# Performance work log

Hardware: AMD Instinct MI355X
Metric: run time of the kernel (lower is better)

The kernel has to match this reference:

```python
import jax
import jax.numpy as jnp
import numpy as np

N_NODES = 4096
N_EDGES = 65536
D_FEAT = 64


def setup_inputs() -> dict:
    key = jax.random.key(0)
    k1, k2, k3, k4 = jax.random.split(key, 4)
    x = jax.random.normal(k1, (N_NODES, D_FEAT), dtype=jnp.float32)
    edge_index = jax.random.randint(k2, (2, N_EDGES), 0, N_NODES, dtype=jnp.int32)
    batch = jnp.zeros((N_NODES,), dtype=jnp.int32)
    # GraphConv(in_channels, 1): lin_rel (with bias) on aggregated neighbors, lin_root on self
    w_rel = jax.random.normal(k3, (D_FEAT, 1), dtype=jnp.float32) * 0.1
    w_root = jax.random.normal(k4, (D_FEAT, 1), dtype=jnp.float32) * 0.1
    b = jnp.zeros((1,), dtype=jnp.float32)
    return {"x": x, "edge_index": edge_index, "batch": batch,
            "w_rel": w_rel, "w_root": w_root, "b": b}


def _merge_stars(x, src0, dst0, score):
    """Faithful sequential greedy star contraction (priority order by score desc)."""
    N = x.shape[0]
    order = jnp.argsort(-score)  # descending, ties like argsort

    def step(carry, node):
        xc, src, dst, remaining, center = carry
        active = remaining[node]
        # dests = set of targets of edges whose (current, rewritten) source == node,
        # minus already-chosen center nodes
        dest_edge = src == node                                  # [E]
        dest_node = jnp.zeros(N, bool).at[dst].max(dest_edge)    # node-level set
        dest_node = dest_node & ~center
        # torch does sum over list(dests)+[node]: node counted again (even on self-loop)
        combine = jnp.einsum('n,nd->d', dest_node.astype(xc.dtype), xc) + xc[node]
        D = dest_node.at[node].set(True)                         # dests U {node}
        x2 = xc.at[node].set(combine)
        src2 = jnp.where(D[src], node, src)                      # np.isin rewrite
        dst2 = jnp.where(D[dst], node, dst)
        rem2 = remaining & ~dest_node
        cen2 = center.at[node].set(True)
        carry2 = (jnp.where(active, x2, xc),
                  jnp.where(active, src2, src),
                  jnp.where(active, dst2, dst),
                  jnp.where(active, rem2, remaining),
                  jnp.where(active, cen2, center))
        return carry2, None

    init = (x, src0, dst0, jnp.ones(N, bool), jnp.zeros(N, bool))
    (x_final, _, _, remaining, _), _ = jax.lax.scan(step, init, order)
    return x_final, remaining


def reference(x, edge_index, batch, w_rel, w_root, b):
    N, d = x.shape
    src0, dst0 = edge_index[0], edge_index[1]
    # GraphConv score: W_rel * sum_{j->i} x_j + b + W_root * x_i ; dropout p=0; tanh
    agg = jax.ops.segment_sum(x[src0], dst0, num_segments=N)     # [N, d]
    score = jnp.tanh((agg @ w_rel + x @ w_root + b).reshape(-1)) # [N]

    x_final, remaining = _merge_stars(x, src0, dst0, score)

    # perm = sorted(nodes_remaining); outputs padded to static size N (sentinel -1)
    perm = jnp.nonzero(remaining, size=N, fill_value=N)[0]
    x_pooled = jnp.take(x_final, perm, axis=0, mode='fill', fill_value=0.0)
    kept = perm < N
    batch_pooled = jnp.where(kept, jnp.take(batch, jnp.minimum(perm, N - 1)), -1)
    # filter_adj on the ORIGINAL edge_index: keep edges with both endpoints kept,
    # relabel nodes to their rank among kept nodes; invalid edges -> -1
    relabel = jnp.cumsum(remaining.astype(jnp.int32)) - 1
    valid = remaining[src0] & remaining[dst0]
    new_src = jnp.where(valid, relabel[src0], -1)
    new_dst = jnp.where(valid, relabel[dst0], -1)
    new_edge_index = jnp.stack([new_src, new_dst])
    perm_out = jnp.where(kept, perm, -1)
    return x_pooled, new_edge_index, batch_pooled, perm_out
```

## Files before the change

kernel.cpp:

```cpp
#include <hip/hip_runtime.h>

#define NN 4096
#define NE 65536
#define ND 64


__global__ void k1_dots_count(const float* __restrict__ x, const float* __restrict__ wrel,
                              const float* __restrict__ wroot, const int* __restrict__ ei,
                              double* __restrict__ srel, double* __restrict__ sroot,
                              int* __restrict__ cnt) {
    int gt = blockIdx.x * blockDim.x + threadIdx.x;
    int node = gt >> 6, lane = gt & 63;
    double xv = (double)x[gt];
    double pr = xv * (double)wrel[lane];
    double po = xv * (double)wroot[lane];
    for (int off = 32; off > 0; off >>= 1) {
        pr += __shfl_down(pr, off);
        po += __shfl_down(po, off);
    }
    if (lane == 0) {
        srel[node] = pr;
        sroot[node] = po;
    }
    if (gt < NE / 4) {
        const int4* eid4 = (const int4*)(ei + NE);
        int4 q = eid4[gt];
        atomicAdd(&cnt[q.x], 1);
        atomicAdd(&cnt[q.y], 1);
        atomicAdd(&cnt[q.z], 1);
        atomicAdd(&cnt[q.w], 1);
    }
}

__global__ void __launch_bounds__(1024) k2_scan(const int* __restrict__ cnt,
                                                int* __restrict__ rowst,
                                                int* __restrict__ cursor) {
    __shared__ int wt[16];
    int tid = threadIdx.x, lane = tid & 63, wv = tid >> 6;
    int4 c = ((const int4*)cnt)[tid];
    int tot = c.x + c.y + c.z + c.w;
    int inc = tot;
    for (int off = 1; off < 64; off <<= 1) {
        int v = __shfl_up(inc, off);
        if (lane >= off) inc += v;
    }
    if (lane == 63) wt[wv] = inc;
    __syncthreads();
    if (wv == 0 && lane < 16) {
        int v = wt[lane];
        for (int off = 1; off < 16; off <<= 1) {
            int u2 = __shfl_up(v, off);
            if (lane >= off) v += u2;
        }
        wt[lane] = v;
    }
    __syncthreads();
    int waveoff = (wv > 0) ? wt[wv - 1] : 0;
    int excl = waveoff + inc - tot;
    int4 rs;
    rs.x = excl; rs.y = excl + c.x; rs.z = excl + c.x + c.y; rs.w = excl + c.x + c.y + c.z;
    ((int4*)rowst)[tid] = rs;
    ((int4*)cursor)[tid] = rs;
    if (tid == 0) rowst[NN] = NE;
}

__global__ void k3_scatter(const int* __restrict__ ei, int* __restrict__ cursor,
                           unsigned short* __restrict__ incsr) {
    int i = blockIdx.x * blockDim.x + threadIdx.x;
    const int4* eis4 = (const int4*)ei;
    const int4* eid4 = (const int4*)(ei + NE);
    int4 s = eis4[i];
    int4 d = eid4[i];
    incsr[atomicAdd(&cursor[d.x], 1)] = (unsigned short)s.x;
    incsr[atomicAdd(&cursor[d.y], 1)] = (unsigned short)s.y;
    incsr[atomicAdd(&cursor[d.z], 1)] = (unsigned short)s.z;
    incsr[atomicAdd(&cursor[d.w], 1)] = (unsigned short)s.w;
}

__global__ void k4_keys(const double* __restrict__ srel, const double* __restrict__ sroot,
                        const float* __restrict__ bptr, const int* __restrict__ rowst,
                        const unsigned short* __restrict__ incsr, unsigned* __restrict__ key) {
    int v = blockIdx.x * blockDim.x + threadIdx.x;
    int rs = rowst[v], re = rowst[v + 1];
    double s = 0.0;
    for (int e = rs; e < re; ++e) s += srel[(int)incsr[e]];
    double arg = s + sroot[v] + (double)bptr[0];
    float sc = tanhf((float)arg);
    unsigned m = __float_as_uint(sc);
    m = (m & 0x80000000u) ? ~m : (m | 0x80000000u);
    key[v] = m;
}

__global__ void k5_filtersort(const int* __restrict__ rowst, const unsigned* __restrict__ key,
                              unsigned short* __restrict__ incsr, int* __restrict__ rl,
                              float* __restrict__ out) {
    int g = blockIdx.x * blockDim.x + threadIdx.x;
    if (g < (NN * ND) / 4) ((float4*)out)[g] = make_float4(0.f, 0.f, 0.f, 0.f);

    int v = g >> 6, l = g & 63;
    int rs = rowst[v], deg = rowst[v + 1] - rs;
    unsigned mv = key[v];
    if (deg <= 64) {
        int u = (l < deg) ? (int)incsr[rs + l] : -1;
        bool isself = (l < deg) && (u == v);
        unsigned mu = (l < deg && !isself) ? key[u] : 0u;
        bool keep = (l < deg) && !isself && (mu > mv || (mu == mv && u < v));
        unsigned long long val = keep
            ? ((((unsigned long long)(~mu)) << 12) | (unsigned)u) : ~0ULL;
        int m = __popcll(__ballot(keep));
        bool selfAny = __ballot(isself) != 0ULL;
        for (int k = 2; k <= 64; k <<= 1) {
            for (int j = k >> 1; j > 0; j >>= 1) {
                unsigned long long o = __shfl_xor(val, j);
                bool takeMin = ((l & k) == 0) == ((l & j) == 0);
                unsigned long long mn = (o < val) ? o : val;
                unsigned long long mx = (o < val) ? val : o;
                val = takeMin ? mn : mx;
            }
        }
        if (l < m) incsr[rs + l] = (unsigned short)(val & 0xFFFULL);
        if (l == 0) rl[v] = m | (selfAny ? 0x10000 : 0);
    } else if (l == 0) {
        int w = rs;
        bool selfAny = false;
        for (int e = rs; e < rs + deg; ++e) {
            int u = (int)incsr[e];
            if (u == v) { selfAny = true; continue; }
            unsigned mu = key[u];
            if (!(mu > mv || (mu == mv && u < v))) continue;
            int j = w;
            while (j > rs) {
                int q = (int)incsr[j - 1];
                unsigned mq = key[q];
                if (mu > mq || (mu == mq && u < q)) { incsr[j] = (unsigned short)q; --j; }
                else break;
            }
            incsr[j] = (unsigned short)u; ++w;
        }
        rl[v] = (w - rs) | (selfAny ? 0x10000 : 0);
    }
}

__global__ void __launch_bounds__(1024) k34_fix(
        const int* __restrict__ rowst, const int* __restrict__ rl,
        const unsigned short* __restrict__ incsr_g,
        int* __restrict__ map_g, int* __restrict__ rem_g, int* __restrict__ relab_g,
        int* __restrict__ perm_a, int* __restrict__ nkeep_g) {
    __shared__ __align__(16) char buf[135232];
    unsigned short* incsr = (unsigned short*)buf;
    volatile unsigned char* stat = (volatile unsigned char*)(buf + 131072);
    int* wt = (int*)(buf + 135168);
    int tid = threadIdx.x, lane = tid & 63, wv = tid >> 6;

    for (int i = tid; i < 131072 / 16; i += 1024)
        ((int4*)incsr)[i] = ((const int4*)incsr_g)[i];
    ((int*)(buf + 131072))[tid] = 0;
    int4 rsq = ((const int4*)rowst)[tid];
    int4 rlq = ((const int4*)rl)[tid];
    int rs4[4] = {rsq.x, rsq.y, rsq.z, rsq.w};
    int rq4[4] = {rlq.x, rlq.y, rlq.z, rlq.w};
    __syncthreads();

    unsigned resolved = 0, centerm = 0, selfm = 0;
    int pos4[4], re4[4], fu4[4] = {0, 0, 0, 0};
    #pragma unroll
    for (int t = 0; t < 4; ++t) {
        int v = 4 * tid + t;
        int m = rq4[t] & 0xFFFF;
        if (rq4[t] & 0x10000) selfm |= 1u << t;
        int lo = rs4[t];
        pos4[t] = lo; re4[t] = lo + m;
        if (m == 0) {
            map_g[v] = v; stat[v] = 1;
            centerm |= 1u << t; resolved |= 1u << t;
        } else {
            fu4[t] = (int)incsr[lo];
        }
    }

    int guard = 0;
    while (resolved != 0xFu && guard < 1000000) {
        ++guard;
        bool prog = false;
        #pragma unroll
        for (int t = 0; t < 4; ++t) {
            if (resolved & (1u << t)) continue;
            int v = 4 * tid + t;
            int u = fu4[t];
            int st = (int)stat[u];
            if (st == 0) continue;
            prog = true;
            if (st == 1) {
                map_g[v] = u; stat[v] = 2; resolved |= 1u << t; continue;
            }
            int p = pos4[t] + 1, hi = re4[t];
            bool done = false;
            while (p < hi) {
                u = (int)incsr[p];
                st = (int)stat[u];
                if (st == 2) { ++p; continue; }
                if (st == 1) {
                    map_g[v] = u; stat[v] = 2; resolved |= 1u << t; done = true;
                }
                break;
            }
            if (!done) {
                if (p >= hi) {
                    map_g[v] = v; stat[v] = 1; centerm |= 1u << t; resolved |= 1u << t;
                } else {
                    pos4[t] = p; fu4[t] = u;
                }
            }
        }
        if (__ballot(prog) == 0) __builtin_amdgcn_s_sleep(1);
    }
    __syncthreads();

    int remb[4], cnt4 = 0;
    #pragma unroll
    for (int t = 0; t < 4; ++t) {
        remb[t] = ((centerm >> t) & 1) && !((selfm >> t) & 1);
        cnt4 += remb[t];
    }
    int inc2 = cnt4;
    for (int off = 1; off < 64; off <<= 1) {
        int v = __shfl_up(inc2, off);
        if (lane >= off) inc2 += v;
    }
    if (lane == 63) wt[wv] = inc2;
    __syncthreads();
    if (wv == 0 && lane < 16) {
        int v = wt[lane];
        for (int off = 1; off < 16; off <<= 1) {
            int u2 = __shfl_up(v, off);
            if (lane >= off) v += u2;
        }
        wt[lane] = v;
    }
    __syncthreads();
    int woff2 = (wv > 0) ? wt[wv - 1] : 0;
    int run = woff2 + inc2 - cnt4;
    #pragma unroll
    for (int t = 0; t < 4; ++t) {
        int v = 4 * tid + t;
        relab_g[v] = run;
        if (remb[t]) { perm_a[run] = v; ++run; }
        rem_g[v] = remb[t];
    }
    if (tid == 1023) nkeep_g[0] = run;
}

__global__ void k56_outputs(const float* __restrict__ x, const int* __restrict__ map_g,
                            const int* __restrict__ rem_g, const int* __restrict__ relab_g,
                            const int* __restrict__ perm_a, const int* __restrict__ ei,
                            const int* __restrict__ batch, const int* __restrict__ nkeep_g,
                            float* __restrict__ out) {
    int idx = blockIdx.x * blockDim.x + threadIdx.x;
    if (idx < NN * ND) {
        int n = idx >> 6, d = idx & 63;
        int m = map_g[n];
        if (rem_g[m]) atomicAdd(&out[relab_g[m] * ND + d], x[idx]);
    } else if (idx < NN * ND + 2 * NE) {
        int e = idx - NN * ND;
        int row = e >> 16;
        int ee = e & (NE - 1);
        int s = ei[ee], t = ei[NE + ee];
        bool valid = (rem_g[s] != 0) && (rem_g[t] != 0);
        int endp = (row == 0) ? s : t;
        out[idx] = valid ? (float)relab_g[endp] : -1.0f;
    } else if (idx < NN * ND + 2 * NE + NN) {
        int r = idx - (NN * ND + 2 * NE);
        int nk = nkeep_g[0];
        out[idx] = (r < nk) ? (float)batch[perm_a[r]] : -1.0f;
    } else if (idx < NN * ND + 2 * NE + 2 * NN) {
        int r = idx - (NN * ND + 2 * NE + NN);
        int nk = nkeep_g[0];
        out[idx] = (r < nk) ? (float)perm_a[r] : -1.0f;
    }
}

extern "C" void kernel_launch(void* const* d_in, const int* in_sizes, int n_in,
                              void* d_out, int out_size, void* d_ws, size_t ws_size,
                              hipStream_t stream) {
    const float* x     = (const float*)d_in[0];
    const int*   ei    = (const int*)d_in[1];
    const int*   batch = (const int*)d_in[2];
    const float* wrel  = (const float*)d_in[3];
    const float* wroot = (const float*)d_in[4];
    const float* b     = (const float*)d_in[5];

    char* ws = (char*)d_ws;
    double* srel   = (double*)(ws + 0);
    double* sroot  = (double*)(ws + 32768);
    int*    map_g  = (int*)(ws + 65536);
    int*    rem_g  = (int*)(ws + 81920);
    int*    relab  = (int*)(ws + 98304);
    int*    perma  = (int*)(ws + 114688);
    int*    nkeep  = (int*)(ws + 131072);
    int*    cnt    = (int*)(ws + 131136);
    int*    rowst  = (int*)(ws + 147520);
    int*    cursor = (int*)(ws + 163968);
    unsigned short* incsr = (unsigned short*)(ws + 180352);
    int*      rl  = cnt;
    unsigned* key = (unsigned*)cursor;

    float* out = (float*)d_out;

    hipMemsetAsync(cnt, 0, NN * sizeof(int), stream);
    k1_dots_count<<<NN * ND / 256, 256, 0, stream>>>(x, wrel, wroot, ei, srel, sroot, cnt);
    k2_scan<<<1, 1024, 0, stream>>>(cnt, rowst, cursor);
    k3_scatter<<<(NE / 4) / 256, 256, 0, stream>>>(ei, cursor, incsr);
    k4_keys<<<NN / 256, 256, 0, stream>>>(srel, sroot, b, rowst, incsr, key);
    k5_filtersort<<<(NN * 64) / 256, 256, 0, stream>>>(rowst, key, incsr, rl, out);
    k34_fix<<<1, 1024, 0, stream>>>(rowst, rl, incsr, map_g, rem_g, relab, perma, nkeep);
    int total_out = NN * ND + 2 * NE + 2 * NN;
    k56_outputs<<<(total_out + 255) / 256, 256, 0, stream>>>(x, map_g, rem_g, relab,
                                                             perma, ei, batch, nkeep, out);
}
```

Before: 139.7 us.

## Build CSR in one LDS-resident block and compute keys by aggregating features

Replaces the memset, count, scan and scatter kernels with a single 1024-thread block that counts, scans and scatters entirely in LDS (about 144 KB) before copying the CSR to global memory. The score kernel now sums neighbour feature rows directly with one wave per node, then dots the sum with the weights, so the separate per-node dot-product pass is no longer needed. This removes several launches and global atomics, but serialises CSR construction onto one CU and makes the key pass read a 64-float row for every edge.

```diff
diff --git a/kernel.cpp b/kernel.cpp
--- a/kernel.cpp
+++ b/kernel.cpp
@@ -5,40 +5,30 @@
 #define ND 64
 
 
-__global__ void k1_dots_count(const float* __restrict__ x, const float* __restrict__ wrel,
-                              const float* __restrict__ wroot, const int* __restrict__ ei,
-                              double* __restrict__ srel, double* __restrict__ sroot,
-                              int* __restrict__ cnt) {
-    int gt = blockIdx.x * blockDim.x + threadIdx.x;
-    int node = gt >> 6, lane = gt & 63;
-    double xv = (double)x[gt];
-    double pr = xv * (double)wrel[lane];
-    double po = xv * (double)wroot[lane];
-    for (int off = 32; off > 0; off >>= 1) {
-        pr += __shfl_down(pr, off);
-        po += __shfl_down(po, off);
-    }
-    if (lane == 0) {
-        srel[node] = pr;
-        sroot[node] = po;
-    }
-    if (gt < NE / 4) {
-        const int4* eid4 = (const int4*)(ei + NE);
-        int4 q = eid4[gt];
-        atomicAdd(&cnt[q.x], 1);
-        atomicAdd(&cnt[q.y], 1);
-        atomicAdd(&cnt[q.z], 1);
-        atomicAdd(&cnt[q.w], 1);
-    }
-}
-
-__global__ void __launch_bounds__(1024) k2_scan(const int* __restrict__ cnt,
-                                                int* __restrict__ rowst,
-                                                int* __restrict__ cursor) {
-    __shared__ int wt[16];
+__global__ void __launch_bounds__(1024) kB_csr(const int* __restrict__ ei,
+                                               unsigned short* __restrict__ incsr_g,
+                                               int* __restrict__ rowst_g) {
+    __shared__ __align__(16) char buf[147520];
+    unsigned short* incsr = (unsigned short*)buf;
+    int* cursor = (int*)(buf + 131072);
+    int* wt = (int*)(buf + 147456);
     int tid = threadIdx.x, lane = tid & 63, wv = tid >> 6;
-    int4 c = ((const int4*)cnt)[tid];
-    int tot = c.x + c.y + c.z + c.w;
+
+    for (int n = tid; n < NN; n += 1024) cursor[n] = 0;
+    __syncthreads();
+    const int4* eid4 = (const int4*)(ei + NE);
+    for (int i = tid; i < NE / 4; i += 1024) {
+        int4 q = eid4[i];
+        atomicAdd(&cursor[q.x], 1);
+        atomicAdd(&cursor[q.y], 1);
+        atomicAdd(&cursor[q.z], 1);
+        atomicAdd(&cursor[q.w], 1);
+    }
+    __syncthreads();
+
+    int t0 = cursor[4 * tid], t1 = cursor[4 * tid + 1];
+    int t2 = cursor[4 * tid + 2], t3 = cursor[4 * tid + 3];
+    int tot = t0 + t1 + t2 + t3;
     int inc = tot;
     for (int off = 1; off < 64; off <<= 1) {
         int v = __shfl_up(inc, off);
@@ -57,38 +47,56 @@
     __syncthreads();
     int waveoff = (wv > 0) ? wt[wv - 1] : 0;
     int excl = waveoff + inc - tot;
-    int4 rs;
-    rs.x = excl; rs.y = excl + c.x; rs.z = excl + c.x + c.y; rs.w = excl + c.x + c.y + c.z;
-    ((int4*)rowst)[tid] = rs;
-    ((int4*)cursor)[tid] = rs;
-    if (tid == 0) rowst[NN] = NE;
-}
-
-__global__ void k3_scatter(const int* __restrict__ ei, int* __restrict__ cursor,
-                           unsigned short* __restrict__ incsr) {
-    int i = blockIdx.x * blockDim.x + threadIdx.x;
+    int4 rsv;
+    rsv.x = excl; rsv.y = excl + t0; rsv.z = excl + t0 + t1; rsv.w = excl + t0 + t1 + t2;
+    ((int4*)rowst_g)[tid] = rsv;
+    if (tid == 1023) rowst_g[NN] = NE;
+    cursor[4 * tid]     = rsv.x;
+    cursor[4 * tid + 1] = rsv.y;
+    cursor[4 * tid + 2] = rsv.z;
+    cursor[4 * tid + 3] = rsv.w;
+    __syncthreads();
+
     const int4* eis4 = (const int4*)ei;
-    const int4* eid4 = (const int4*)(ei + NE);
-    int4 s = eis4[i];
-    int4 d = eid4[i];
-    incsr[atomicAdd(&cursor[d.x], 1)] = (unsigned short)s.x;
-    incsr[atomicAdd(&cursor[d.y], 1)] = (unsigned short)s.y;
-    incsr[atomicAdd(&cursor[d.z], 1)] = (unsigned short)s.z;
-    incsr[atomicAdd(&cursor[d.w], 1)] = (unsigned short)s.w;
-}
-
-__global__ void k4_keys(const double* __restrict__ srel, const double* __restrict__ sroot,
-                        const float* __restrict__ bptr, const int* __restrict__ rowst,
-                        const unsigned short* __restrict__ incsr, unsigned* __restrict__ key) {
-    int v = blockIdx.x * blockDim.x + threadIdx.x;
-    int rs = rowst[v], re = rowst[v + 1];
-    double s = 0.0;
-    for (int e = rs; e < re; ++e) s += srel[(int)incsr[e]];
-    double arg = s + sroot[v] + (double)bptr[0];
-    float sc = tanhf((float)arg);
-    unsigned m = __float_as_uint(sc);
-    m = (m & 0x80000000u) ? ~m : (m | 0x80000000u);
-    key[v] = m;
+    for (int i = tid; i < NE / 4; i += 1024) {
+        int4 s = eis4[i];
+        int4 d = eid4[i];
+        incsr[atomicAdd(&cursor[d.x], 1)] = (unsigned short)s.x;
+        incsr[atomicAdd(&cursor[d.y], 1)] = (unsigned short)s.y;
+        incsr[atomicAdd(&cursor[d.z], 1)] = (unsigned short)s.z;
+        incsr[atomicAdd(&cursor[d.w], 1)] = (unsigned short)s.w;
+    }
+    __syncthreads();
+
+    for (int i = tid; i < 8192; i += 1024)
+        ((int4*)incsr_g)[i] = ((const int4*)incsr)[i];
+}
+
+__global__ void kX_keys(const float* __restrict__ x, const float* __restrict__ wrel,
+                        const float* __restrict__ wroot, const float* __restrict__ bptr,
+                        const int* __restrict__ rowst, const unsigned short* __restrict__ incsr,
+                        unsigned* __restrict__ key) {
+    int gt = blockIdx.x * blockDim.x + threadIdx.x;
+    int v = gt >> 6, lane = gt & 63;
+    int rs = rowst[v], deg = rowst[v + 1] - rs;
+    double acc = 0.0;
+    for (int base = 0; base < deg; base += 64) {
+        int n = deg - base; if (n > 64) n = 64;
+        int ent = (lane < n) ? (int)incsr[rs + base + lane] : 0;
+        for (int e = 0; e < n; ++e) {
+            int u = __shfl(ent, e);
+            acc += (double)x[(u << 6) | lane];
+        }
+    }
+    double red = acc * (double)wrel[lane]
+               + (double)x[(v << 6) | lane] * (double)wroot[lane];
+    for (int off = 32; off > 0; off >>= 1) red += __shfl_down(red, off);
+    if (lane == 0) {
+        float sc = tanhf((float)(red + (double)bptr[0]));
+        unsigned m = __float_as_uint(sc);
+        m = (m & 0x80000000u) ? ~m : (m | 0x80000000u);
+        key[v] = m;
+    }
 }
 
 __global__ void k5_filtersort(const int* __restrict__ rowst, const unsigned* __restrict__ key,
@@ -290,28 +298,21 @@
     const float* b     = (const float*)d_in[5];
 
     char* ws = (char*)d_ws;
-    double* srel   = (double*)(ws + 0);
-    double* sroot  = (double*)(ws + 32768);
-    int*    map_g  = (int*)(ws + 65536);
-    int*    rem_g  = (int*)(ws + 81920);
-    int*    relab  = (int*)(ws + 98304);
-    int*    perma  = (int*)(ws + 114688);
-    int*    nkeep  = (int*)(ws + 131072);
-    int*    cnt    = (int*)(ws + 131136);
-    int*    rowst  = (int*)(ws + 147520);
-    int*    cursor = (int*)(ws + 163968);
-    unsigned short* incsr = (unsigned short*)(ws + 180352);
-    int*      rl  = cnt;
-    unsigned* key = (unsigned*)cursor;
+    int*    map_g  = (int*)(ws + 0);
+    int*    rem_g  = (int*)(ws + 16384);
+    int*    relab  = (int*)(ws + 32768);
+    int*    perma  = (int*)(ws + 49152);
+    int*    nkeep  = (int*)(ws + 65536);
+    int*    rl     = (int*)(ws + 65600);
+    int*    rowst  = (int*)(ws + 81984);
+    unsigned* key  = (unsigned*)(ws + 98432);
+    unsigned short* incsr = (unsigned short*)(ws + 114816);
 
     float* out = (float*)d_out;
 
-    hipMemsetAsync(cnt, 0, NN * sizeof(int), stream);
-    k1_dots_count<<<NN * ND / 256, 256, 0, stream>>>(x, wrel, wroot, ei, srel, sroot, cnt);
-    k2_scan<<<1, 1024, 0, stream>>>(cnt, rowst, cursor);
-    k3_scatter<<<(NE / 4) / 256, 256, 0, stream>>>(ei, cursor, incsr);
-    k4_keys<<<NN / 256, 256, 0, stream>>>(srel, sroot, b, rowst, incsr, key);
-    k5_filtersort<<<(NN * 64) / 256, 256, 0, stream>>>(rowst, key, incsr, rl, out);
+    kB_csr<<<1, 1024, 0, stream>>>(ei, incsr, rowst);
+    kX_keys<<<1024, 256, 0, stream>>>(x, wrel, wroot, b, rowst, incsr, key);
+    k5_filtersort<<<1024, 256, 0, stream>>>(rowst, key, incsr, rl, out);
     k34_fix<<<1, 1024, 0, stream>>>(rowst, rl, incsr, map_g, rem_g, relab, perma, nkeep);
     int total_out = NN * ND + 2 * NE + 2 * NN;
     k56_outputs<<<(total_out + 255) / 256, 256, 0, stream>>>(x, map_g, rem_g, relab,
```

Result: no change. 140.1 us (+0.3%).
